# Kernel optimization log

Measured on AMD Instinct MI355X. Metric: run time of the kernel, lower is better.

Reference implementation:

```python
import jax, jax.numpy as jnp
import numpy as np

N_NODES = 50000
N_EDGES = 800000
IN_FEAT = 128
HEADS = 8
HEAD_DIM = 16  # out_feat // num_heads = 128 // 8
NEG_SLOPE = 0.2


def setup_inputs() -> dict:
    key = jax.random.key(0)
    ks = jax.random.split(key, 8)
    g = 1.0 / np.sqrt(IN_FEAT)
    return {
        "x": jax.random.normal(ks[0], (N_NODES, IN_FEAT), jnp.float32),
        "efeat": jax.random.normal(ks[1], (N_EDGES, IN_FEAT), jnp.float32),
        "src": jax.random.randint(ks[2], (N_EDGES,), 0, N_NODES),
        "dst": jax.random.randint(ks[3], (N_EDGES,), 0, N_NODES),
        "W_src": jax.random.normal(ks[4], (HEADS * HEAD_DIM, IN_FEAT), jnp.float32) * g,
        "b_src": jnp.zeros((HEADS * HEAD_DIM,), jnp.float32),
        "W_dst": jax.random.normal(ks[5], (HEADS * HEAD_DIM, IN_FEAT), jnp.float32) * g,
        "b_dst": jnp.zeros((HEADS * HEAD_DIM,), jnp.float32),
        "W_edge": jax.random.normal(ks[6], (HEADS * HEAD_DIM, IN_FEAT), jnp.float32) * g,
        "attn": jax.random.normal(ks[7], (HEADS, HEAD_DIM), jnp.float32) * (1.0 / np.sqrt(HEAD_DIM)),
    }


def reference(x, efeat, src, dst, W_src, b_src, W_dst, b_dst, W_edge, attn):
    H, D = HEADS, HEAD_DIM
    # node/edge projections: [N,H,D] / [E,H,D]
    feat_src = (x @ W_src.T + b_src).reshape(-1, H, D)
    feat_dst = (x @ W_dst.T + b_dst).reshape(-1, H, D)
    feat_edge = (efeat @ W_edge.T).reshape(-1, H, D)

    # per-edge GATv2 score: LeakyReLU(src + dst + edge) . attn  -> [E,H]
    fs = feat_src[src]                                    # gather [E,H,D]
    tmp = fs + feat_dst[dst] + feat_edge
    e = jnp.where(tmp >= 0, tmp, NEG_SLOPE * tmp)
    score = jnp.einsum('ehd,hd->eh', e, attn)

    # edge softmax normalized per destination node
    m = jax.ops.segment_max(score, dst, num_segments=N_NODES)     # [N,H]
    ex = jnp.exp(score - jax.lax.stop_gradient(m)[dst])
    z = jax.ops.segment_sum(ex, dst, num_segments=N_NODES)        # [N,H]
    a = ex / z[dst]                                               # [E,H]

    # weighted scatter-sum of (src + edge) messages
    msg = (fs + feat_edge) * a[:, :, None]                        # [E,H,D]
    h = jax.ops.segment_sum(msg, dst, num_segments=N_NODES)       # [N,H,D]

    # res_fc is None since in_feat == H*D; activation = relu
    h = jax.nn.relu(h)
    return h.reshape(N_NODES, H * D)
```

## Files before the change

### kernel.cpp

```cpp
#include <hip/hip_runtime.h>
#include <hip/hip_bf16.h>

#define NNODES 50000
#define NEDGES 800000
#define NEG_SLOPE 0.2f
#define N_PAD 50176

typedef float f32x4 __attribute__((ext_vector_type(4)));
typedef float f32x2 __attribute__((ext_vector_type(2)));
typedef __bf16 bf16x8 __attribute__((ext_vector_type(8)));
typedef __bf16 bf16x4 __attribute__((ext_vector_type(4)));
typedef __bf16 bf16x2 __attribute__((ext_vector_type(2)));

__global__ __launch_bounds__(256) void convert_w3(
    const float* __restrict__ W0, const float* __restrict__ W1,
    const float* __restrict__ W2, __bf16* __restrict__ out)
{
  int m = blockIdx.x >> 4;
  const float* W = (m == 0) ? W0 : ((m == 1) ? W1 : W2);
  __bf16* o = out + m * 16384;
  int i = (blockIdx.x & 15) * 1024 + threadIdx.x * 4;
  int r = i >> 7, cx = i & 127;
  f32x4 v = *(const f32x4*)(W + i);
  int kb = cx >> 3, ko = cx & 7;
  int off = r * 128 + ((kb ^ (r & 15)) << 3) + ko;
  bf16x4 pk = { (__bf16)v.x, (__bf16)v.y, (__bf16)v.z, (__bf16)v.w };
  *(bf16x4*)(o + off) = pk;
}

template<int OUT_BF16, int HAS_BIAS, int SCATTER>
__global__ __launch_bounds__(256, 2) void gemm_proj(
    const float* __restrict__ A, const __bf16* __restrict__ Wsw,
    const float* __restrict__ bias, const int* __restrict__ rank,
    void* __restrict__ outp, int M)
{
  __shared__ __bf16 sS[128 * 136];
  const int t = threadIdx.x;
  const int m0 = blockIdx.x * 128;

  #pragma unroll
  for (int it = 0; it < 8; ++it) {
    int lin = it * 2048 + t * 8;
    *(bf16x8*)(sS + lin) = *(const bf16x8*)(Wsw + lin);
  }

  const int w = t >> 6, lane = t & 63;
  const int rsel = lane & 15, quad = lane >> 4;

  f32x4 raw[16];
  #pragma unroll
  for (int mi = 0; mi < 2; ++mi) {
    int gr = m0 + w * 32 + mi * 16 + rsel;
    const float* p = A + (size_t)gr * 128 + (quad << 3);
    bool ok = gr < M;
    #pragma unroll
    for (int kk = 0; kk < 4; ++kk) {
      f32x4 z4 = {0.f, 0.f, 0.f, 0.f};
      raw[mi * 8 + kk * 2]     = ok ? *(const f32x4*)(p + kk * 32)     : z4;
      raw[mi * 8 + kk * 2 + 1] = ok ? *(const f32x4*)(p + kk * 32 + 4) : z4;
    }
  }
  bf16x8 af[4][2];
  #pragma unroll
  for (int kk = 0; kk < 4; ++kk)
    #pragma unroll
    for (int mi = 0; mi < 2; ++mi) {
      f32x4 v0 = raw[mi * 8 + kk * 2], v1 = raw[mi * 8 + kk * 2 + 1];
      af[kk][mi] = (bf16x8){ (__bf16)v0.x, (__bf16)v0.y, (__bf16)v0.z, (__bf16)v0.w,
                             (__bf16)v1.x, (__bf16)v1.y, (__bf16)v1.z, (__bf16)v1.w };
    }

  f32x4 acc[2][8];
  f32x4 zero = {0.f, 0.f, 0.f, 0.f};
  #pragma unroll
  for (int mi = 0; mi < 2; ++mi)
    #pragma unroll
    for (int ni = 0; ni < 8; ++ni) acc[mi][ni] = zero;

  __syncthreads();

  #pragma unroll
  for (int kk = 0; kk < 4; ++kk) {
    int kb0 = kk * 4 + quad;
    bf16x8 bfr[8];
    #pragma unroll
    for (int ni = 0; ni < 8; ++ni) {
      int r = ni * 16 + rsel;
      bfr[ni] = *(const bf16x8*)(sS + r * 128 + ((kb0 ^ (r & 15)) << 3));
    }
    #pragma unroll
    for (int mi = 0; mi < 2; ++mi)
      #pragma unroll
      for (int ni = 0; ni < 8; ++ni)
        acc[mi][ni] = __builtin_amdgcn_mfma_f32_16x16x32_bf16(af[kk][mi], bfr[ni], acc[mi][ni], 0, 0, 0);
  }

  if (OUT_BF16 && SCATTER) {
    __syncthreads();
    #pragma unroll
    for (int mi = 0; mi < 2; ++mi)
      #pragma unroll
      for (int ni = 0; ni < 8; ++ni)
        #pragma unroll
        for (int r4 = 0; r4 < 4; ++r4) {
          float v = acc[mi][ni][r4];
          float vx = __shfl_xor(v, 1);
          if (!(rsel & 1)) {
            int trow = w * 32 + mi * 16 + quad * 4 + r4;
            bf16x2 pkv = { (__bf16)v, (__bf16)vx };
            *(bf16x2*)(sS + trow * 136 + ni * 16 + rsel) = pkv;
          }
        }
    __syncthreads();
    int tr = t >> 1, h = t & 1;
    int grow = m0 + tr;
    if (grow < M) {
      int orw = rank[grow];
      const __bf16* sp = sS + tr * 136 + h * 64;
      __bf16* dp = (__bf16*)outp + (size_t)orw * 128 + h * 64;
      #pragma unroll
      for (int i = 0; i < 8; ++i)
        *(bf16x8*)(dp + i * 8) = *(const bf16x8*)(sp + i * 8);
    }
  } else {
    #pragma unroll
    for (int mi = 0; mi < 2; ++mi)
      #pragma unroll
      for (int ni = 0; ni < 8; ++ni)
        #pragma unroll
        for (int r4 = 0; r4 < 4; ++r4) {
          int grow = m0 + w * 32 + mi * 16 + quad * 4 + r4;
          int col = ni * 16 + rsel;
          if (grow < M) {
            float v = acc[mi][ni][r4];
            if (HAS_BIAS) v += bias[col];
            ((float*)outp)[(size_t)grow * 128 + col] = v;
          }
        }
  }
}

__global__ void hist_kernel(const int* __restrict__ dst, int* __restrict__ deg,
                            int* __restrict__ arr){
  int e = blockIdx.x * 256 + threadIdx.x;
  arr[e] = atomicAdd(&deg[dst[e]], 1);
}

__global__ void scan_local(const int* __restrict__ deg, int* __restrict__ scanned,
                           int* __restrict__ bsum){
  __shared__ int s[1024];
  int t = threadIdx.x, i = blockIdx.x * 1024 + t;
  int v = deg[i];
  s[t] = v; __syncthreads();
  #pragma unroll
  for (int off = 1; off < 1024; off <<= 1){
    int x = (t >= off) ? s[t - off] : 0;
    __syncthreads();
    s[t] += x;
    __syncthreads();
  }
  scanned[i] = s[t] - v;
  if (t == 1023) bsum[blockIdx.x] = s[t];
}

__global__ void scan_sums(int* __restrict__ bsum){
  __shared__ int s[64];
  int t = threadIdx.x;
  int v = (t < 49) ? bsum[t] : 0;
  s[t] = v; __syncthreads();
  #pragma unroll
  for (int off = 1; off < 64; off <<= 1){
    int x = (t >= off) ? s[t - off] : 0;
    __syncthreads();
    s[t] += x;
    __syncthreads();
  }
  bsum[t] = s[t] - v;
}

__global__ void scan_add(const int* __restrict__ scanned, const int* __restrict__ bsum,
                         int* __restrict__ row_start){
  int i = blockIdx.x * 256 + threadIdx.x;
  if (i < N_PAD) row_start[i] = scanned[i] + bsum[i >> 10];
}

__global__ void scatter_kernel(const int* __restrict__ dst, const int* __restrict__ src,
                               const int* __restrict__ row_start, int* __restrict__ rank,
                               int* __restrict__ src_perm){
  int e = blockIdx.x * 256 + threadIdx.x;
  int pos = row_start[dst[e]] + rank[e];
  rank[e] = pos;
  src_perm[pos] = src[e];
}

__global__ __launch_bounds__(256) void aggregate_fused(
    const int* __restrict__ row_start, const int* __restrict__ deg,
    const int* __restrict__ src_perm, const float* __restrict__ fs,
    const float* __restrict__ fd, const __bf16* __restrict__ fe,
    const float* __restrict__ attn, float* __restrict__ out)
{
  int wv = threadIdx.x >> 6, lane = threadIdx.x & 63;
  int n = blockIdx.x * 4 + wv;
  int row = row_start[n], dg = deg[n];
  int c = lane << 1;
  f32x2 fdv = *(const f32x2*)(fd + (size_t)n * 128 + c);
  f32x2 atv = *(const f32x2*)(attn + c);
  float acc0 = 0.f, acc1 = 0.f, zs = 0.f;
  const __bf16* fep = fe + (size_t)row * 128 + c;

  #define EDGE_BODY(FV, EV)                                            \
    {                                                                  \
      float v0 = (FV).x + (float)(EV).x;                               \
      float v1 = (FV).y + (float)(EV).y;                               \
      float t0 = v0 + fdv.x; t0 = t0 >= 0.f ? t0 : NEG_SLOPE * t0;     \
      float t1 = v1 + fdv.y; t1 = t1 >= 0.f ? t1 : NEG_SLOPE * t1;     \
      float p = t0 * atv.x + t1 * atv.y;                               \
      p += __shfl_xor(p, 1);                                           \
      p += __shfl_xor(p, 2);                                           \
      p += __shfl_xor(p, 4);                                           \
      float ex = __expf(p);                                            \
      acc0 += ex * v0; acc1 += ex * v1; zs += ex;                      \
    }

  for (int base = 0; base < dg; base += 64){
    int cnt = min(64, dg - base);
    int si = 0;
    if (lane < cnt) si = src_perm[row + base + lane];
    int j = 0;
    for (; j + 4 <= cnt; j += 4){
      int s0 = __shfl(si, j,     64);
      int s1 = __shfl(si, j + 1, 64);
      int s2 = __shfl(si, j + 2, 64);
      int s3 = __shfl(si, j + 3, 64);
      f32x2 f0 = *(const f32x2*)(fs + (size_t)s0 * 128 + c);
      f32x2 f1 = *(const f32x2*)(fs + (size_t)s1 * 128 + c);
      f32x2 f2 = *(const f32x2*)(fs + (size_t)s2 * 128 + c);
      f32x2 f3 = *(const f32x2*)(fs + (size_t)s3 * 128 + c);
      bf16x2 e0 = *(const bf16x2*)(fep + (size_t)(base + j)     * 128);
      bf16x2 e1 = *(const bf16x2*)(fep + (size_t)(base + j + 1) * 128);
      bf16x2 e2 = *(const bf16x2*)(fep + (size_t)(base + j + 2) * 128);
      bf16x2 e3 = *(const bf16x2*)(fep + (size_t)(base + j + 3) * 128);
      EDGE_BODY(f0, e0)
      EDGE_BODY(f1, e1)
      EDGE_BODY(f2, e2)
      EDGE_BODY(f3, e3)
    }
    for (; j < cnt; ++j){
      int s0 = __shfl(si, j, 64);
      f32x2 f0 = *(const f32x2*)(fs + (size_t)s0 * 128 + c);
      bf16x2 e0 = *(const bf16x2*)(fep + (size_t)(base + j) * 128);
      EDGE_BODY(f0, e0)
    }
  }
  #undef EDGE_BODY

  float rz = zs > 0.f ? 1.f / zs : 0.f;
  float o0 = acc0 * rz, o1 = acc1 * rz;
  f32x2 ov = { o0 > 0.f ? o0 : 0.f, o1 > 0.f ? o1 : 0.f };
  *(f32x2*)(out + (size_t)n * 128 + c) = ov;
}

extern "C" void kernel_launch(void* const* d_in, const int* in_sizes, int n_in,
                              void* d_out, int out_size, void* d_ws, size_t ws_size,
                              hipStream_t stream)
{
  const float* x      = (const float*)d_in[0];
  const float* efeat  = (const float*)d_in[1];
  const int*   src    = (const int*)d_in[2];
  const int*   dst    = (const int*)d_in[3];
  const float* W_src  = (const float*)d_in[4];
  const float* b_src  = (const float*)d_in[5];
  const float* W_dst  = (const float*)d_in[6];
  const float* b_dst  = (const float*)d_in[7];
  const float* W_edge = (const float*)d_in[8];
  const float* attn   = (const float*)d_in[9];

  char* ws = (char*)d_ws;
  float*  feat_src  = (float*)(ws + 0);
  float*  feat_dst  = (float*)(ws + 25600000);
  __bf16* fe        = (__bf16*)(ws + 51200000);
  int*    src_perm  = (int*)  (ws + 256000000);
  int*    rank      = (int*)  (ws + 259200000);
  int*    row_start = (int*)  (ws + 262400000);
  int*    scanned   = (int*)  (ws + 262801408);
  int*    deg       = (int*)  (ws + 263002112);
  int*    bsum      = (int*)  (ws + 263202816);
  __bf16* wsw       = (__bf16*)(ws + 263203840);

  hipMemsetAsync(deg, 0, 200704, stream);

  convert_w3<<<48, 256, 0, stream>>>(W_src, W_dst, W_edge, wsw);

  hist_kernel   <<<3125, 256, 0, stream>>>(dst, deg, rank);
  scan_local    <<<49, 1024, 0, stream>>>(deg, scanned, bsum);
  scan_sums     <<<1, 64, 0, stream>>>(bsum);
  scan_add      <<<196, 256, 0, stream>>>(scanned, bsum, row_start);
  scatter_kernel<<<3125, 256, 0, stream>>>(dst, src, row_start, rank, src_perm);

  gemm_proj<0,1,0><<<391, 256, 0, stream>>>(x, wsw,           b_src, nullptr, feat_src, NNODES);
  gemm_proj<0,1,0><<<391, 256, 0, stream>>>(x, wsw + 16384,   b_dst, nullptr, feat_dst, NNODES);
  gemm_proj<1,0,1><<<6250, 256, 0, stream>>>(efeat, wsw + 32768, nullptr, rank, fe, NEDGES);

  aggregate_fused<<<12500, 256, 0, stream>>>(row_start, deg, src_perm, feat_src,
                                             feat_dst, fe, attn, (float*)d_out);
}
```

Measured before the change: 792.4 us.

## Merge small kernels into fewer launches and fuse three projection GEMMs

```diff
diff --git a/kernel.cpp b/kernel.cpp
--- a/kernel.cpp
+++ b/kernel.cpp
@@ -12,31 +12,37 @@
 typedef __bf16 bf16x4 __attribute__((ext_vector_type(4)));
 typedef __bf16 bf16x2 __attribute__((ext_vector_type(2)));
 
-__global__ __launch_bounds__(256) void convert_w3(
+__global__ __launch_bounds__(256) void convert_hist(
     const float* __restrict__ W0, const float* __restrict__ W1,
-    const float* __restrict__ W2, __bf16* __restrict__ out)
-{
-  int m = blockIdx.x >> 4;
-  const float* W = (m == 0) ? W0 : ((m == 1) ? W1 : W2);
-  __bf16* o = out + m * 16384;
-  int i = (blockIdx.x & 15) * 1024 + threadIdx.x * 4;
-  int r = i >> 7, cx = i & 127;
-  f32x4 v = *(const f32x4*)(W + i);
-  int kb = cx >> 3, ko = cx & 7;
-  int off = r * 128 + ((kb ^ (r & 15)) << 3) + ko;
-  bf16x4 pk = { (__bf16)v.x, (__bf16)v.y, (__bf16)v.z, (__bf16)v.w };
-  *(bf16x4*)(o + off) = pk;
+    const float* __restrict__ W2, __bf16* __restrict__ out,
+    const int* __restrict__ dst, int* __restrict__ deg, int* __restrict__ arr)
+{
+  int b = blockIdx.x;
+  if (b < 48) {
+    int m = b >> 4;
+    const float* W = (m == 0) ? W0 : ((m == 1) ? W1 : W2);
+    __bf16* o = out + m * 16384;
+    int i = (b & 15) * 1024 + threadIdx.x * 4;
+    int r = i >> 7, cx = i & 127;
+    f32x4 v = *(const f32x4*)(W + i);
+    int kb = cx >> 3, ko = cx & 7;
+    int off = r * 128 + ((kb ^ (r & 15)) << 3) + ko;
+    bf16x4 pk = { (__bf16)v.x, (__bf16)v.y, (__bf16)v.z, (__bf16)v.w };
+    *(bf16x4*)(o + off) = pk;
+  } else {
+    int e = (b - 48) * 256 + threadIdx.x;
+    arr[e] = atomicAdd(&deg[dst[e]], 1);
+  }
 }
 
 template<int OUT_BF16, int HAS_BIAS, int SCATTER>
-__global__ __launch_bounds__(256, 2) void gemm_proj(
-    const float* __restrict__ A, const __bf16* __restrict__ Wsw,
+__device__ __forceinline__ void gemm_body(
+    int tile, const float* __restrict__ A, const __bf16* __restrict__ Wsw,
     const float* __restrict__ bias, const int* __restrict__ rank,
-    void* __restrict__ outp, int M)
-{
-  __shared__ __bf16 sS[128 * 136];
+    void* __restrict__ outp, int M, __bf16* sS)
+{
   const int t = threadIdx.x;
-  const int m0 = blockIdx.x * 128;
+  const int m0 = tile * 128;
 
   #pragma unroll
   for (int it = 0; it < 8; ++it) {
@@ -47,28 +53,24 @@
   const int w = t >> 6, lane = t & 63;
   const int rsel = lane & 15, quad = lane >> 4;
 
-  f32x4 raw[16];
+  bf16x8 af[4][2];
   #pragma unroll
   for (int mi = 0; mi < 2; ++mi) {
     int gr = m0 + w * 32 + mi * 16 + rsel;
     const float* p = A + (size_t)gr * 128 + (quad << 3);
     bool ok = gr < M;
+    f32x4 r0[4], r1[4];
     #pragma unroll
     for (int kk = 0; kk < 4; ++kk) {
       f32x4 z4 = {0.f, 0.f, 0.f, 0.f};
-      raw[mi * 8 + kk * 2]     = ok ? *(const f32x4*)(p + kk * 32)     : z4;
-      raw[mi * 8 + kk * 2 + 1] = ok ? *(const f32x4*)(p + kk * 32 + 4) : z4;
-    }
-  }
-  bf16x8 af[4][2];
-  #pragma unroll
-  for (int kk = 0; kk < 4; ++kk)
-    #pragma unroll
-    for (int mi = 0; mi < 2; ++mi) {
-      f32x4 v0 = raw[mi * 8 + kk * 2], v1 = raw[mi * 8 + kk * 2 + 1];
-      af[kk][mi] = (bf16x8){ (__bf16)v0.x, (__bf16)v0.y, (__bf16)v0.z, (__bf16)v0.w,
-                             (__bf16)v1.x, (__bf16)v1.y, (__bf16)v1.z, (__bf16)v1.w };
-    }
+      r0[kk] = ok ? *(const f32x4*)(p + kk * 32)     : z4;
+      r1[kk] = ok ? *(const f32x4*)(p + kk * 32 + 4) : z4;
+    }
+    #pragma unroll
+    for (int kk = 0; kk < 4; ++kk)
+      af[kk][mi] = (bf16x8){ (__bf16)r0[kk].x, (__bf16)r0[kk].y, (__bf16)r0[kk].z, (__bf16)r0[kk].w,
+                             (__bf16)r1[kk].x, (__bf16)r1[kk].y, (__bf16)r1[kk].z, (__bf16)r1[kk].w };
+  }
 
   f32x4 acc[2][8];
   f32x4 zero = {0.f, 0.f, 0.f, 0.f};
@@ -140,10 +142,21 @@
   }
 }
 
-__global__ void hist_kernel(const int* __restrict__ dst, int* __restrict__ deg,
-                            int* __restrict__ arr){
-  int e = blockIdx.x * 256 + threadIdx.x;
-  arr[e] = atomicAdd(&deg[dst[e]], 1);
+__global__ __launch_bounds__(256, 4) void proj_all(
+    const float* __restrict__ x, const float* __restrict__ efeat,
+    const __bf16* __restrict__ wsw, const float* __restrict__ b_src,
+    const float* __restrict__ b_dst, const int* __restrict__ rank,
+    float* __restrict__ feat_src, float* __restrict__ feat_dst,
+    __bf16* __restrict__ fe)
+{
+  __shared__ __bf16 sS[128 * 136];
+  int b = blockIdx.x;
+  if (b < 6250)
+    gemm_body<1,0,1>(b, efeat, wsw + 32768, nullptr, rank, fe, NEDGES, sS);
+  else if (b < 6641)
+    gemm_body<0,1,0>(b - 6250, x, wsw, b_src, nullptr, feat_src, NNODES, sS);
+  else
+    gemm_body<0,1,0>(b - 6641, x, wsw + 16384, b_dst, nullptr, feat_dst, NNODES, sS);
 }
 
 __global__ void scan_local(const int* __restrict__ deg, int* __restrict__ scanned,
@@ -163,25 +176,18 @@
   if (t == 1023) bsum[blockIdx.x] = s[t];
 }
 
-__global__ void scan_sums(int* __restrict__ bsum){
-  __shared__ int s[64];
-  int t = threadIdx.x;
-  int v = (t < 49) ? bsum[t] : 0;
-  s[t] = v; __syncthreads();
-  #pragma unroll
-  for (int off = 1; off < 64; off <<= 1){
-    int x = (t >= off) ? s[t - off] : 0;
-    __syncthreads();
-    s[t] += x;
-    __syncthreads();
-  }
-  bsum[t] = s[t] - v;
-}
-
 __global__ void scan_add(const int* __restrict__ scanned, const int* __restrict__ bsum,
                          int* __restrict__ row_start){
-  int i = blockIdx.x * 256 + threadIdx.x;
-  if (i < N_PAD) row_start[i] = scanned[i] + bsum[i >> 10];
+  __shared__ int sbase;
+  int b = blockIdx.x, t = threadIdx.x;
+  if (t == 0){
+    int lim = b >> 2, acc = 0;
+    for (int j = 0; j < lim; ++j) acc += bsum[j];
+    sbase = acc;
+  }
+  __syncthreads();
+  int i = b * 256 + t;
+  if (i < N_PAD) row_start[i] = scanned[i] + sbase;
 }
 
 __global__ void scatter_kernel(const int* __restrict__ dst, const int* __restrict__ src,
@@ -289,17 +295,14 @@
 
   hipMemsetAsync(deg, 0, 200704, stream);
 
-  convert_w3<<<48, 256, 0, stream>>>(W_src, W_dst, W_edge, wsw);
-
-  hist_kernel   <<<3125, 256, 0, stream>>>(dst, deg, rank);
+  convert_hist<<<3173, 256, 0, stream>>>(W_src, W_dst, W_edge, wsw, dst, deg, rank);
+
   scan_local    <<<49, 1024, 0, stream>>>(deg, scanned, bsum);
-  scan_sums     <<<1, 64, 0, stream>>>(bsum);
   scan_add      <<<196, 256, 0, stream>>>(scanned, bsum, row_start);
   scatter_kernel<<<3125, 256, 0, stream>>>(dst, src, row_start, rank, src_perm);
 
-  gemm_proj<0,1,0><<<391, 256, 0, stream>>>(x, wsw,           b_src, nullptr, feat_src, NNODES);
-  gemm_proj<0,1,0><<<391, 256, 0, stream>>>(x, wsw + 16384,   b_dst, nullptr, feat_dst, NNODES);
-  gemm_proj<1,0,1><<<6250, 256, 0, stream>>>(efeat, wsw + 32768, nullptr, rank, fe, NEDGES);
+  proj_all<<<7032, 256, 0, stream>>>(x, efeat, wsw, b_src, b_dst, rank,
+                                     feat_src, feat_dst, fe);
 
   aggregate_fused<<<12500, 256, 0, stream>>>(row_start, deg, src_perm, feat_src,
                                              feat_dst, fe, attn, (float*)d_out);
```

Result: faster. 770.8 us (-2.7%).
